# Kernel optimization log

Hardware: AMD Instinct MI355X
Metric: run time of the kernel (lower is better)

## Reference

```python
import jax, jax.numpy as jnp
import numpy as np

N = 50000        # nodes
E = 800000       # edges per meta-path (avg degree 16)
M = 3            # meta-paths
IN = 256         # in_size
HID = 16         # hidden_size (per-head out dim of GATConv)
HEADS = 8
OUT = 8          # out_size (classes)
SA_HID = 128     # StructureAttention hidden_size default
NEG_SLOPE = 0.2  # DGL GATConv leaky_relu default


def setup_inputs() -> dict:
    key = jax.random.key(0)
    ks = jax.random.split(key, 11)
    h = jax.random.normal(ks[0], (N, IN), jnp.float32)
    edges = jax.random.randint(ks[1], (M, 2, E), 0, N, jnp.int32)  # [M, (src,dst), E]
    s = 0.05
    fc_w = jax.random.normal(ks[2], (M, IN, HEADS * HID), jnp.float32) * s
    attn_l = jax.random.normal(ks[3], (M, HEADS, HID), jnp.float32) * s
    attn_r = jax.random.normal(ks[4], (M, HEADS, HID), jnp.float32) * s
    sa_w1 = jax.random.normal(ks[5], (HEADS * HID, SA_HID), jnp.float32) * s
    sa_b1 = jnp.zeros((SA_HID,), jnp.float32)
    sa_w2 = jax.random.normal(ks[6], (SA_HID, 1), jnp.float32) * s
    pred_w = jax.random.normal(ks[7], (HEADS * HID, OUT), jnp.float32) * s
    pred_b = jnp.zeros((OUT,), jnp.float32)
    return {"h": h, "edges": edges, "fc_w": fc_w, "attn_l": attn_l,
            "attn_r": attn_r, "sa_w1": sa_w1, "sa_b1": sa_b1, "sa_w2": sa_w2,
            "pred_w": pred_w, "pred_b": pred_b}


def _gat(h, src, dst, w, al, ar):
    # DGL GATConv, eval mode (dropout=0), activation=elu
    feat = (h @ w).reshape(N, HEADS, HID)                 # [N,H,D]
    el = jnp.einsum('nhd,hd->nh', feat, al)               # [N,H]
    er = jnp.einsum('nhd,hd->nh', feat, ar)               # [N,H]
    e = el[src] + er[dst]                                 # [E,H]
    e = jnp.where(e > 0, e, NEG_SLOPE * e)                # leaky_relu
    # edge softmax over incoming edges of each dst node
    emax = jax.ops.segment_max(e, dst, num_segments=N)    # [N,H]
    ex = jnp.exp(e - emax[dst])                           # [E,H]
    denom = jax.ops.segment_sum(ex, dst, num_segments=N)  # [N,H]
    alpha = ex / denom[dst]                               # [E,H]
    msg = feat[src] * alpha[:, :, None]                   # [E,H,D]
    out = jax.ops.segment_sum(msg, dst, num_segments=N)   # [N,H,D]
    return jax.nn.elu(out).reshape(N, HEADS * HID)        # flatten(1)


def reference(h, edges, fc_w, attn_l, attn_r, sa_w1, sa_b1, sa_w2, pred_w, pred_b):
    # per-meta-path GAT (loop over fixed small set of meta-paths)
    zs = [_gat(h, edges[i, 0], edges[i, 1], fc_w[i], attn_l[i], attn_r[i])
          for i in range(M)]
    z = jnp.stack(zs, axis=1)                             # [N, M, H*D]
    # StructureAttention exactly as in source: softmax over dim 0 (nodes)
    w = jnp.tanh(z @ sa_w1 + sa_b1) @ sa_w2               # [N, M, 1]
    beta = jax.nn.softmax(w, axis=0)                      # softmax over nodes
    fused = (beta * z).sum(0)                             # [M, H*D]
    return fused @ pred_w + pred_b                        # [M, OUT]
```

## Files before the change

kernel.cpp:

```cpp
#include <hip/hip_runtime.h>

#define N_NODES 50000
#define N_EDGES 800000
#define N_META 3
#define IN_DIM 256
#define HD 128
#define HEADS 8
#define HID 16
#define OUT_DIM 8
#define NBKT 196
#define BCAP 5120
#define TILE_E 4096
#define GEMM_BX ((N_NODES + 31) / 32)
#define WG_BX   ((N_NODES + 63) / 64)
#define ELER_BX ((N_NODES * HEADS + 255) / 256)
#define BING_NB (3 * NBKT)
#define PSTRIDE 132

using bf16x8 = __attribute__((ext_vector_type(8))) short;
using f32x4  = __attribute__((ext_vector_type(4))) float;

__device__ __forceinline__ float bf2f(unsigned short u) {
  union { unsigned int i; float f; } x; x.i = ((unsigned int)u) << 16; return x.f;
}
__device__ __forceinline__ unsigned short f2bf(float f) {
  union { float f; unsigned int i; } x; x.f = f;
  unsigned int r = x.i + 0x7fffu + ((x.i >> 16) & 1u);
  return (unsigned short)(r >> 16);
}
__device__ __forceinline__ float tanh_fast(float x) {
  float e = __expf(2.f * x);
  return 1.f - 2.f / (e + 1.f);
}

__global__ __launch_bounds__(256)
void prep_kernel(const float* __restrict__ fcw, const float* __restrict__ w1,
                 unsigned short* __restrict__ fcwT, unsigned short* __restrict__ w1T,
                 int* __restrict__ gcur) {
  int i = blockIdx.x * 256 + threadIdx.x;
  const int NFC = N_META * IN_DIM * HD;
  const int NW1 = HD * HD;
  const int NGC = N_META * NBKT;
  if (i < NFC) {
    int p = i / (IN_DIM * HD);
    int rem = i - p * (IN_DIM * HD);
    int k = rem / HD, n = rem - k * HD;
    fcwT[(size_t)p * HD * IN_DIM + n * IN_DIM + k] = f2bf(fcw[i]);
  } else if (i < NFC + NW1) {
    int j = i - NFC;
    int k = j / HD, n = j - k * HD;
    w1T[n * HD + k] = f2bf(w1[j]);
  } else if (i < NFC + NW1 + NGC) {
    gcur[i - NFC - NW1] = 0;
  }
}

__global__ __launch_bounds__(256)
void bin_kernel(const int* __restrict__ edges, int* __restrict__ gcur,
                unsigned int* __restrict__ bktbuf) {
  __shared__ int hist[NBKT];
  __shared__ int gbase[NBKT];
  __shared__ int fill[NBKT];
  int t = threadIdx.x;
  int bx = blockIdx.x;
  int p = bx / NBKT;
  int b = bx - p * NBKT;
  int e0 = b * TILE_E;
  const int* src = edges + (size_t)p * 2 * N_EDGES;
  const int* dst = src + N_EDGES;
  for (int i = t; i < NBKT; i += 256) { hist[i] = 0; fill[i] = 0; }
  __syncthreads();
  for (int i = t; i < TILE_E; i += 256) {
    int e = e0 + i;
    if (e < N_EDGES) atomicAdd(&hist[dst[e] >> 8], 1);
  }
  __syncthreads();
  for (int i = t; i < NBKT; i += 256) {
    int idx = p * NBKT + i;
    gbase[i] = hist[i] ? (idx * BCAP + atomicAdd(&gcur[idx], hist[i])) : 0;
  }
  __syncthreads();
  for (int i = t; i < TILE_E; i += 256) {
    int e = e0 + i;
    if (e < N_EDGES) {
      int d = dst[e];
      int b2 = d >> 8;
      int r = atomicAdd(&fill[b2], 1);
      bktbuf[gbase[b2] + r] = ((unsigned int)(d & 255) << 16) | (unsigned int)src[e];
    }
  }
}

__global__ __launch_bounds__(256)
void gemm_kernel(const float* __restrict__ A,
                 const unsigned short* __restrict__ BT,
                 unsigned short* __restrict__ Cb, int nrows) {
  int t = threadIdx.x;
  int w = t >> 6, l = t & 63, q = l >> 4, s = l & 15;
  int row0 = blockIdx.x * 32;
  const unsigned short* Bw = BT + (size_t)(w * 96) * IN_DIM;
  int gr0 = min(row0 + s,      nrows - 1);
  int gr1 = min(row0 + 16 + s, nrows - 1);
  const float* ap0 = A + (size_t)gr0 * IN_DIM + q * 8;
  const float* ap1 = A + (size_t)gr1 * IN_DIM + q * 8;
  f32x4 acc[2][6] = {};
  #pragma unroll 2
  for (int kc = 0; kc < 8; ++kc) {
    int k0 = kc * 32;
    bf16x8 af[2];
    {
      float4 a0 = *(const float4*)(ap0 + k0);
      float4 a1 = *(const float4*)(ap0 + k0 + 4);
      union { bf16x8 v; ushort4 u[2]; } cv;
      ushort4 u0, u1;
      u0.x = f2bf(a0.x); u0.y = f2bf(a0.y); u0.z = f2bf(a0.z); u0.w = f2bf(a0.w);
      u1.x = f2bf(a1.x); u1.y = f2bf(a1.y); u1.z = f2bf(a1.z); u1.w = f2bf(a1.w);
      cv.u[0] = u0; cv.u[1] = u1;
      af[0] = cv.v;
    }
    {
      float4 a0 = *(const float4*)(ap1 + k0);
      float4 a1 = *(const float4*)(ap1 + k0 + 4);
      union { bf16x8 v; ushort4 u[2]; } cv;
      ushort4 u0, u1;
      u0.x = f2bf(a0.x); u0.y = f2bf(a0.y); u0.z = f2bf(a0.z); u0.w = f2bf(a0.w);
      u1.x = f2bf(a1.x); u1.y = f2bf(a1.y); u1.z = f2bf(a1.z); u1.w = f2bf(a1.w);
      cv.u[0] = u0; cv.u[1] = u1;
      af[1] = cv.v;
    }
    bf16x8 bfv[6];
    #pragma unroll
    for (int nt = 0; nt < 6; ++nt)
      bfv[nt] = *(const bf16x8*)(Bw + (size_t)(nt * 16 + s) * IN_DIM + k0 + q * 8);
    #pragma unroll
    for (int mt = 0; mt < 2; ++mt) {
      #pragma unroll
      for (int nt = 0; nt < 6; ++nt)
        acc[mt][nt] = __builtin_amdgcn_mfma_f32_16x16x32_bf16(af[mt], bfv[nt], acc[mt][nt], 0, 0, 0);
    }
  }
  #pragma unroll
  for (int mt = 0; mt < 2; ++mt) {
    #pragma unroll
    for (int nt = 0; nt < 6; ++nt) {
      int gc = w * 96 + nt * 16 + s;
      int mm = gc >> 7, cim = gc & 127;
      unsigned short* Cm = Cb + (size_t)mm * N_NODES * HD;
      #pragma unroll
      for (int r = 0; r < 4; ++r) {
        int gr = row0 + mt * 16 + q * 4 + r;
        if (gr < nrows) Cm[(size_t)gr * HD + cim] = f2bf(acc[mt][nt][r]);
      }
    }
  }
}

__global__ __launch_bounds__(256)
void sort_eler_kernel(const int* __restrict__ gcur,
                      const unsigned int* __restrict__ bktbuf,
                      int* __restrict__ offsB, int* __restrict__ offsE,
                      int* __restrict__ csr,
                      const unsigned short* __restrict__ featb3,
                      const float* __restrict__ al, const float* __restrict__ ar,
                      float* __restrict__ el3, float* __restrict__ er3) {
  __shared__ int lh[256];
  __shared__ int cur[256];
  __shared__ int wsum[4];
  int p = blockIdx.y;
  int t = threadIdx.x;
  if (blockIdx.x < NBKT) {
    int b = blockIdx.x;
    int lane = t & 63, wid = t >> 6;
    int idx = p * NBKT + b;
    int S = idx * BCAP;
    int E = S + gcur[idx];
    int node0 = b * 256;
    int nn = min(256, N_NODES - node0);
    int gi0 = p * N_NODES + node0;
    lh[t] = 0;
    __syncthreads();
    for (int i = S + t; i < E; i += 256) atomicAdd(&lh[bktbuf[i] >> 16], 1);
    __syncthreads();
    int v = lh[t];
    int s = v;
    #pragma unroll
    for (int d = 1; d < 64; d <<= 1) {
      int x = __shfl_up(s, d);
      if (lane >= d) s += x;
    }
    if (lane == 63) wsum[wid] = s;
    __syncthreads();
    int woff = 0;
    #pragma unroll
    for (int k = 0; k < 4; ++k) if (k < wid) woff += wsum[k];
    int excl = S + woff + s - v;
    if (t < nn) {
      offsB[gi0 + t] = excl;
      offsE[gi0 + t] = excl + v;
    }
    cur[t] = excl;
    __syncthreads();
    for (int i = S + t; i < E; i += 256) {
      unsigned int rec = bktbuf[i];
      int pos = atomicAdd(&cur[rec >> 16], 1);
      csr[pos] = (int)(rec & 0xffffu);
    }
  } else {
    int i = (blockIdx.x - NBKT) * 256 + t;
    if (i >= N_NODES * HEADS) return;
    int node = i >> 3, hh = i & 7;
    const unsigned short* f =
        featb3 + (size_t)p * N_NODES * HD + (size_t)node * HD + hh * HID;
    uint4 u0 = *(const uint4*)(f);
    uint4 u1 = *(const uint4*)(f + 8);
    unsigned int uu[8] = {u0.x, u0.y, u0.z, u0.w, u1.x, u1.y, u1.z, u1.w};
    const float* alm = al + p * HD + hh * HID;
    const float* arm = ar + p * HD + hh * HID;
    float sl = 0.f, sr = 0.f;
    #pragma unroll
    for (int q = 0; q < 8; ++q) {
      float v0 = __uint_as_float(uu[q] << 16);
      float v1 = __uint_as_float(uu[q] & 0xffff0000u);
      int d = q * 2;
      sl += v0 * alm[d] + v1 * alm[d + 1];
      sr += v0 * arm[d] + v1 * arm[d + 1];
    }
    el3[(size_t)p * N_NODES * HEADS + i] = sl;
    er3[(size_t)p * N_NODES * HEADS + i] = sr;
  }
}

__global__ __launch_bounds__(256)
void aggregate_kernel(const int* __restrict__ offsB3, const int* __restrict__ offsE3,
                      const int* __restrict__ csr,
                      const uint4* __restrict__ featb3_u4,
                      const float* __restrict__ el3, const float* __restrict__ er3,
                      uint4* __restrict__ zb3_u4, int m) {
  int node = blockIdx.x * 4 + (threadIdx.x >> 6);
  if (node >= N_NODES) return;
  const uint4* featb_u4 = featb3_u4 + (size_t)m * N_NODES * 16;
  const float* el = el3 + (size_t)m * N_NODES * HEADS;
  const float* er = er3 + (size_t)m * N_NODES * HEADS;
  uint4* z_u4 = zb3_u4 + (size_t)m * N_NODES * 16;
  int lane = threadIdx.x & 63;
  int qg = lane >> 4;
  int li = lane & 15;
  int ch = li >> 1;
  int beg = offsB3[m * N_NODES + node], end = offsE3[m * N_NODES + node];
  float erh = er[node * HEADS + ch];
  float ssum = 0.f;
  float a[8] = {};
  for (int i = beg; i < end; i += 16) {
    int nk = end - i;
    int last = end - 1;
    int s0 = csr[min(i + qg,      last)];
    int s1 = csr[min(i + qg + 4,  last)];
    int s2 = csr[min(i + qg + 8,  last)];
    int s3 = csr[min(i + qg + 12, last)];
    uint4 v0 = featb_u4[(size_t)s0 * 16 + li];
    uint4 v1 = featb_u4[(size_t)s1 * 16 + li];
    uint4 v2 = featb_u4[(size_t)s2 * 16 + li];
    uint4 v3 = featb_u4[(size_t)s3 * 16 + li];
    float e0 = el[s0 * HEADS + ch] + erh;
    float e1 = el[s1 * HEADS + ch] + erh;
    float e2 = el[s2 * HEADS + ch] + erh;
    float e3 = el[s3 * HEADS + ch] + erh;
    e0 = e0 > 0.f ? e0 : 0.2f * e0;
    e1 = e1 > 0.f ? e1 : 0.2f * e1;
    e2 = e2 > 0.f ? e2 : 0.2f * e2;
    e3 = e3 > 0.f ? e3 : 0.2f * e3;
    float w0 = (qg      < nk) ? __expf(e0) : 0.f;
    float w1 = (qg + 4  < nk) ? __expf(e1) : 0.f;
    float w2 = (qg + 8  < nk) ? __expf(e2) : 0.f;
    float w3 = (qg + 12 < nk) ? __expf(e3) : 0.f;
    ssum += (w0 + w1) + (w2 + w3);
    a[0] += w0 * __uint_as_float(v0.x << 16);
    a[1] += w0 * __uint_as_float(v0.x & 0xffff0000u);
    a[2] += w0 * __uint_as_float(v0.y << 16);
    a[3] += w0 * __uint_as_float(v0.y & 0xffff0000u);
    a[4] += w0 * __uint_as_float(v0.z << 16);
    a[5] += w0 * __uint_as_float(v0.z & 0xffff0000u);
    a[6] += w0 * __uint_as_float(v0.w << 16);
    a[7] += w0 * __uint_as_float(v0.w & 0xffff0000u);
    a[0] += w1 * __uint_as_float(v1.x << 16);
    a[1] += w1 * __uint_as_float(v1.x & 0xffff0000u);
    a[2] += w1 * __uint_as_float(v1.y << 16);
    a[3] += w1 * __uint_as_float(v1.y & 0xffff0000u);
    a[4] += w1 * __uint_as_float(v1.z << 16);
    a[5] += w1 * __uint_as_float(v1.z & 0xffff0000u);
    a[6] += w1 * __uint_as_float(v1.w << 16);
    a[7] += w1 * __uint_as_float(v1.w & 0xffff0000u);
    a[0] += w2 * __uint_as_float(v2.x << 16);
    a[1] += w2 * __uint_as_float(v2.x & 0xffff0000u);
    a[2] += w2 * __uint_as_float(v2.y << 16);
    a[3] += w2 * __uint_as_float(v2.y & 0xffff0000u);
    a[4] += w2 * __uint_as_float(v2.z << 16);
    a[5] += w2 * __uint_as_float(v2.z & 0xffff0000u);
    a[6] += w2 * __uint_as_float(v2.w << 16);
    a[7] += w2 * __uint_as_float(v2.w & 0xffff0000u);
    a[0] += w3 * __uint_as_float(v3.x << 16);
    a[1] += w3 * __uint_as_float(v3.x & 0xffff0000u);
    a[2] += w3 * __uint_as_float(v3.y << 16);
    a[3] += w3 * __uint_as_float(v3.y & 0xffff0000u);
    a[4] += w3 * __uint_as_float(v3.z << 16);
    a[5] += w3 * __uint_as_float(v3.z & 0xffff0000u);
    a[6] += w3 * __uint_as_float(v3.w << 16);
    a[7] += w3 * __uint_as_float(v3.w & 0xffff0000u);
  }
  #pragma unroll
  for (int j = 0; j < 8; ++j) {
    a[j] += __shfl_xor(a[j], 16);
    a[j] += __shfl_xor(a[j], 32);
  }
  ssum += __shfl_xor(ssum, 16);
  ssum += __shfl_xor(ssum, 32);
  float inv = (end > beg) ? 1.f / ssum : 0.f;
  if (qg == 0) {
    #pragma unroll
    for (int j = 0; j < 8; ++j) {
      float z = a[j] * inv;
      a[j] = z > 0.f ? z : __expf(z) - 1.f;
    }
    uint4 o;
    unsigned int p0, p1, p2, p3;
    asm("v_cvt_pk_bf16_f32 %0, %1, %2" : "=v"(p0) : "v"(a[0]), "v"(a[1]));
    asm("v_cvt_pk_bf16_f32 %0, %1, %2" : "=v"(p1) : "v"(a[2]), "v"(a[3]));
    asm("v_cvt_pk_bf16_f32 %0, %1, %2" : "=v"(p2) : "v"(a[4]), "v"(a[5]));
    asm("v_cvt_pk_bf16_f32 %0, %1, %2" : "=v"(p3) : "v"(a[6]), "v"(a[7]));
    o.x = p0; o.y = p1; o.z = p2; o.w = p3;
    z_u4[(size_t)node * 16 + li] = o;
  }
}

__global__ __launch_bounds__(256)
void w_gemm_mfma(const unsigned short* __restrict__ Zb3,
                 const unsigned short* __restrict__ BT,
                 const float* __restrict__ B1, const float* __restrict__ W2,
                 float* __restrict__ partial, int nrows) {
  __shared__ unsigned short Bs[128 * 128];
  __shared__ float ew[64];
  __shared__ float part[4][64][2];
  int tid = threadIdx.x;
  int m = blockIdx.y;
  const unsigned short* Zb = Zb3 + (size_t)m * N_NODES * HD;
  int w = tid >> 6, l = tid & 63, q = l >> 4, s = l & 15;
  int row0 = blockIdx.x * 64;
  {
    int n = tid >> 1;
    int jb = (tid & 1) * 8;
    #pragma unroll
    for (int jj = 0; jj < 8; ++jj) {
      int j = jb + jj;
      *(uint4*)&Bs[n * 128 + ((j ^ (n & 15)) << 3)] =
          *(const uint4*)(BT + n * HD + j * 8);
    }
  }
  float b1v[8], w2v[8];
  #pragma unroll
  for (int f = 0; f < 8; ++f) { b1v[f] = B1[f * 16 + s]; w2v[f] = W2[f * 16 + s]; }
  int gra = min(row0 + w * 16 + s, nrows - 1);
  const unsigned short* arow = Zb + (size_t)gra * HD;
  bf16x8 af[4];
  #pragma unroll
  for (int kc = 0; kc < 4; ++kc)
    af[kc] = *(const bf16x8*)(arow + kc * 32 + q * 8);
  __syncthreads();
  f32x4 acc[8] = {};
  #pragma unroll
  for (int kc = 0; kc < 4; ++kc) {
    #pragma unroll
    for (int f = 0; f < 8; ++f) {
      bf16x8 bf = *(bf16x8*)&Bs[(f * 16 + s) * 128 + ((((kc << 2) | q) ^ s) << 3)];
      acc[f] = __builtin_amdgcn_mfma_f32_16x16x32_bf16(af[kc], bf, acc[f], 0, 0, 0);
    }
  }
  #pragma unroll
  for (int r = 0; r < 4; ++r) {
    float p = 0.f;
    #pragma unroll
    for (int f = 0; f < 8; ++f) p += tanh_fast(acc[f][r] + b1v[f]) * w2v[f];
    p += __shfl_xor(p, 1); p += __shfl_xor(p, 2);
    p += __shfl_xor(p, 4); p += __shfl_xor(p, 8);
    if (s == 0) {
      int rr = w * 16 + q * 4 + r;
      ew[rr] = (row0 + rr < nrows) ? __expf(p) : 0.f;
    }
  }
  __syncthreads();
  const unsigned int* Zu = (const unsigned int*)Zb;
  int rmax = min(64, nrows - row0);
  float a0 = 0.f, a1 = 0.f;
  for (int r = w; r < rmax; r += 4) {
    float e = ew[r];
    unsigned int v = Zu[(size_t)(row0 + r) * 64 + l];
    a0 += e * __uint_as_float(v << 16);
    a1 += e * __uint_as_float(v & 0xffff0000u);
  }
  part[w][l][0] = a0;
  part[w][l][1] = a1;
  __syncthreads();
  if (w == 0) {
    float s0 = part[0][l][0] + part[1][l][0] + part[2][l][0] + part[3][l][0];
    float s1 = part[0][l][1] + part[1][l][1] + part[2][l][1] + part[3][l][1];
    float* prow = partial + ((size_t)m * WG_BX + blockIdx.x) * PSTRIDE;
    prow[2 * l]     = s0;
    prow[2 * l + 1] = s1;
    float ldv = ew[l];
    ldv += __shfl_xor(ldv, 1);  ldv += __shfl_xor(ldv, 2);
    ldv += __shfl_xor(ldv, 4);  ldv += __shfl_xor(ldv, 8);
    ldv += __shfl_xor(ldv, 16); ldv += __shfl_xor(ldv, 32);
    if (l == 0) prow[128] = ldv;
  }
}

__global__ __launch_bounds__(256)
void reduce_final_kernel(const float* __restrict__ partial,
                         const float* __restrict__ PW, const float* __restrict__ PB,
                         float* __restrict__ out) {
  __shared__ float num[129];
  int m = blockIdx.x;
  int t = threadIdx.x;
  if (t < 129) {
    const float* base = partial + (size_t)m * WG_BX * PSTRIDE + t;
    float a0 = 0.f, a1 = 0.f, a2 = 0.f, a3 = 0.f;
    int b = 0;
    for (; b + 4 <= WG_BX; b += 4) {
      a0 += base[(size_t)(b + 0) * PSTRIDE];
      a1 += base[(size_t)(b + 1) * PSTRIDE];
      a2 += base[(size_t)(b + 2) * PSTRIDE];
      a3 += base[(size_t)(b + 3) * PSTRIDE];
    }
    for (; b < WG_BX; ++b) a0 += base[(size_t)b * PSTRIDE];
    num[t] = (a0 + a1) + (a2 + a3);
  }
  __syncthreads();
  if (t < OUT_DIM) {
    float inv = 1.f / num[128];
    float s = 0.f;
    for (int k = 0; k < HD; ++k) s += num[k] * PW[k * OUT_DIM + t];
    out[m * OUT_DIM + t] = s * inv + PB[t];
  }
}

extern "C" void kernel_launch(void* const* d_in, const int* in_sizes, int n_in,
                              void* d_out, int out_size, void* d_ws, size_t ws_size,
                              hipStream_t stream) {
  (void)in_sizes; (void)n_in; (void)out_size; (void)ws_size;
  const float* h     = (const float*)d_in[0];
  const int*   edges = (const int*)d_in[1];
  const float* fcw   = (const float*)d_in[2];
  const float* al    = (const float*)d_in[3];
  const float* ar    = (const float*)d_in[4];
  const float* w1    = (const float*)d_in[5];
  const float* b1    = (const float*)d_in[6];
  const float* w2    = (const float*)d_in[7];
  const float* pw    = (const float*)d_in[8];
  const float* pb    = (const float*)d_in[9];
  float* out = (float*)d_out;

  char* ws = (char*)d_ws;
  size_t off = 0;
  auto alloc = [&](size_t bytes) -> void* {
    void* p = ws + off;
    off = (off + bytes + 255) & ~(size_t)255;
    return p;
  };
  unsigned short* featb3 = (unsigned short*)alloc((size_t)N_META * N_NODES * HD * 2);
  unsigned short* zb3    = (unsigned short*)alloc((size_t)N_META * N_NODES * HD * 2);
  unsigned short* fcwT   = (unsigned short*)alloc((size_t)N_META * HD * IN_DIM * 2);
  unsigned short* w1T    = (unsigned short*)alloc((size_t)HD * HD * 2);
  float* el3 = (float*)alloc((size_t)N_META * N_NODES * HEADS * 4);
  float* er3 = (float*)alloc((size_t)N_META * N_NODES * HEADS * 4);
  int* gcur  = (int*)alloc((size_t)N_META * NBKT * 4);
  int* offsB = (int*)alloc((size_t)N_META * N_NODES * 4);
  int* offsE = (int*)alloc((size_t)N_META * N_NODES * 4);
  unsigned int* bktbuf = (unsigned int*)alloc((size_t)N_META * NBKT * BCAP * 4);
  int* csr   = (int*)alloc((size_t)N_META * NBKT * BCAP * 4);
  float* partial = (float*)alloc((size_t)N_META * WG_BX * PSTRIDE * 4);

  const int PREP_N = N_META * IN_DIM * HD + HD * HD + N_META * NBKT;
  prep_kernel<<<(PREP_N + 255) / 256, 256, 0, stream>>>(
      fcw, w1, fcwT, w1T, gcur);

  bin_kernel<<<BING_NB, 256, 0, stream>>>(edges, gcur, bktbuf);
  gemm_kernel<<<GEMM_BX, 256, 0, stream>>>(h, fcwT, featb3, N_NODES);

  dim3 bgrid_(NBKT + ELER_BX, N_META);
  sort_eler_kernel<<<bgrid_, 256, 0, stream>>>(
      gcur, bktbuf, offsB, offsE, csr, featb3, al, ar, el3, er3);

  for (int mm = 0; mm < N_META; ++mm) {
    aggregate_kernel<<<(N_NODES + 3) / 4, 256, 0, stream>>>(
        offsB, offsE, csr, (const uint4*)featb3, el3, er3, (uint4*)zb3, mm);
  }

  dim3 wgrid((N_NODES + 63) / 64, N_META);
  w_gemm_mfma<<<wgrid, 256, 0, stream>>>(zb3, w1T, b1, w2, partial, N_NODES);

  reduce_final_kernel<<<N_META, 256, 0, stream>>>(partial, pw, pb, out);
}
```

Baseline: 377.3 us.

## Restructure feature GEMM as persistent grid with register-resident weight tiles per meta-path

After: 401.7 us. +6.5%, slower.

```diff
diff --git a/kernel.cpp b/kernel.cpp
--- a/kernel.cpp
+++ b/kernel.cpp
@@ -11,7 +11,7 @@
 #define NBKT 196
 #define BCAP 5120
 #define TILE_E 4096
-#define GEMM_BX ((N_NODES + 31) / 32)
+#define GEMM_BX 391
 #define WG_BX   ((N_NODES + 63) / 64)
 #define ELER_BX ((N_NODES * HEADS + 255) / 256)
 #define BING_NB (3 * NBKT)
@@ -97,59 +97,40 @@
                  unsigned short* __restrict__ Cb, int nrows) {
   int t = threadIdx.x;
   int w = t >> 6, l = t & 63, q = l >> 4, s = l & 15;
-  int row0 = blockIdx.x * 32;
-  const unsigned short* Bw = BT + (size_t)(w * 96) * IN_DIM;
-  int gr0 = min(row0 + s,      nrows - 1);
-  int gr1 = min(row0 + 16 + s, nrows - 1);
-  const float* ap0 = A + (size_t)gr0 * IN_DIM + q * 8;
-  const float* ap1 = A + (size_t)gr1 * IN_DIM + q * 8;
-  f32x4 acc[2][6] = {};
-  #pragma unroll 2
+  int m = blockIdx.y;
+  const unsigned short* Bm = BT + (size_t)m * HD * IN_DIM;
+  int c0 = w * 32;
+  bf16x8 bfv[8][2];
+  #pragma unroll
   for (int kc = 0; kc < 8; ++kc) {
-    int k0 = kc * 32;
-    bf16x8 af[2];
-    {
-      float4 a0 = *(const float4*)(ap0 + k0);
-      float4 a1 = *(const float4*)(ap0 + k0 + 4);
+    #pragma unroll
+    for (int nt = 0; nt < 2; ++nt)
+      bfv[kc][nt] = *(const bf16x8*)(
+          Bm + (size_t)(c0 + nt * 16 + s) * IN_DIM + kc * 32 + q * 8);
+  }
+  unsigned short* Cm = Cb + (size_t)m * N_NODES * HD;
+  for (int row0 = blockIdx.x * 16; row0 < nrows; row0 += GEMM_BX * 16) {
+    int gr = min(row0 + s, nrows - 1);
+    const float* ap = A + (size_t)gr * IN_DIM + q * 8;
+    f32x4 acc[2] = {};
+    #pragma unroll
+    for (int kc = 0; kc < 8; ++kc) {
+      float4 a0 = *(const float4*)(ap + kc * 32);
+      float4 a1 = *(const float4*)(ap + kc * 32 + 4);
       union { bf16x8 v; ushort4 u[2]; } cv;
       ushort4 u0, u1;
       u0.x = f2bf(a0.x); u0.y = f2bf(a0.y); u0.z = f2bf(a0.z); u0.w = f2bf(a0.w);
       u1.x = f2bf(a1.x); u1.y = f2bf(a1.y); u1.z = f2bf(a1.z); u1.w = f2bf(a1.w);
       cv.u[0] = u0; cv.u[1] = u1;
-      af[0] = cv.v;
-    }
-    {
-      float4 a0 = *(const float4*)(ap1 + k0);
-      float4 a1 = *(const float4*)(ap1 + k0 + 4);
-      union { bf16x8 v; ushort4 u[2]; } cv;
-      ushort4 u0, u1;
-      u0.x = f2bf(a0.x); u0.y = f2bf(a0.y); u0.z = f2bf(a0.z); u0.w = f2bf(a0.w);
-      u1.x = f2bf(a1.x); u1.y = f2bf(a1.y); u1.z = f2bf(a1.z); u1.w = f2bf(a1.w);
-      cv.u[0] = u0; cv.u[1] = u1;
-      af[1] = cv.v;
-    }
-    bf16x8 bfv[6];
-    #pragma unroll
-    for (int nt = 0; nt < 6; ++nt)
-      bfv[nt] = *(const bf16x8*)(Bw + (size_t)(nt * 16 + s) * IN_DIM + k0 + q * 8);
-    #pragma unroll
-    for (int mt = 0; mt < 2; ++mt) {
-      #pragma unroll
-      for (int nt = 0; nt < 6; ++nt)
-        acc[mt][nt] = __builtin_amdgcn_mfma_f32_16x16x32_bf16(af[mt], bfv[nt], acc[mt][nt], 0, 0, 0);
-    }
-  }
-  #pragma unroll
-  for (int mt = 0; mt < 2; ++mt) {
-    #pragma unroll
-    for (int nt = 0; nt < 6; ++nt) {
-      int gc = w * 96 + nt * 16 + s;
-      int mm = gc >> 7, cim = gc & 127;
-      unsigned short* Cm = Cb + (size_t)mm * N_NODES * HD;
+      acc[0] = __builtin_amdgcn_mfma_f32_16x16x32_bf16(cv.v, bfv[kc][0], acc[0], 0, 0, 0);
+      acc[1] = __builtin_amdgcn_mfma_f32_16x16x32_bf16(cv.v, bfv[kc][1], acc[1], 0, 0, 0);
+    }
+    #pragma unroll
+    for (int nt = 0; nt < 2; ++nt) {
       #pragma unroll
       for (int r = 0; r < 4; ++r) {
-        int gr = row0 + mt * 16 + q * 4 + r;
-        if (gr < nrows) Cm[(size_t)gr * HD + cim] = f2bf(acc[mt][nt][r]);
+        int grow = row0 + q * 4 + r;
+        if (grow < nrows) Cm[(size_t)grow * HD + c0 + nt * 16 + s] = f2bf(acc[nt][r]);
       }
     }
   }
@@ -483,7 +464,8 @@
       fcw, w1, fcwT, w1T, gcur);
 
   bin_kernel<<<BING_NB, 256, 0, stream>>>(edges, gcur, bktbuf);
-  gemm_kernel<<<GEMM_BX, 256, 0, stream>>>(h, fcwT, featb3, N_NODES);
+  dim3 ggrid_(GEMM_BX, N_META);
+  gemm_kernel<<<ggrid_, 256, 0, stream>>>(h, fcwT, featb3, N_NODES);
 
   dim3 bgrid_(NBKT + ELER_BX, N_META);
   sort_eler_kernel<<<bgrid_, 256, 0, stream>>>(
```
